# Kernel tuning notes

Hardware: AMD Instinct MI355X
Metric: run time of the kernel (lower is better)

## Reference

```python
import jax, jax.numpy as jnp
import numpy as np

NUM_HEADS = 16
DIM_EMBED = 1024
DIM_CROSS = 768
DIM_HEAD = DIM_EMBED // NUM_HEADS


def setup_inputs() -> dict:
    key = jax.random.key(0)
    ks = jax.random.split(key, 10)
    B, Sq, Skv = 16, 4096, 77
    s_e = 1.0 / np.sqrt(DIM_EMBED)
    s_c = 1.0 / np.sqrt(DIM_CROSS)
    return {
        "x": jax.random.normal(ks[0], (B, Sq, DIM_EMBED), jnp.float32),
        "y": jax.random.normal(ks[1], (B, Skv, DIM_CROSS), jnp.float32),
        "wq": jax.random.uniform(ks[2], (DIM_EMBED, DIM_EMBED), jnp.float32, -s_e, s_e),
        "bq": jax.random.uniform(ks[3], (DIM_EMBED,), jnp.float32, -s_e, s_e),
        "wk": jax.random.uniform(ks[4], (DIM_CROSS, DIM_EMBED), jnp.float32, -s_c, s_c),
        "bk": jax.random.uniform(ks[5], (DIM_EMBED,), jnp.float32, -s_c, s_c),
        "wv": jax.random.uniform(ks[6], (DIM_CROSS, DIM_EMBED), jnp.float32, -s_c, s_c),
        "bv": jax.random.uniform(ks[7], (DIM_EMBED,), jnp.float32, -s_c, s_c),
        "wo": jax.random.uniform(ks[8], (DIM_EMBED, DIM_EMBED), jnp.float32, -s_e, s_e),
        "bo": jax.random.uniform(ks[9], (DIM_EMBED,), jnp.float32, -s_e, s_e),
    }


def reference(x, y, wq, bq, wk, bk, wv, bv, wo, bo):
    B, Sq, E = x.shape
    H, D = NUM_HEADS, DIM_HEAD
    q = (x @ wq + bq).reshape(B, Sq, H, D).transpose(0, 2, 1, 3)   # [B,H,Sq,D]
    k = (y @ wk + bk).reshape(B, -1, H, D).transpose(0, 2, 1, 3)   # [B,H,Skv,D]
    v = (y @ wv + bv).reshape(B, -1, H, D).transpose(0, 2, 1, 3)   # [B,H,Skv,D]
    scale = 1.0 / jnp.sqrt(jnp.asarray(D, dtype=q.dtype))
    scores = jnp.einsum("bhqd,bhkd->bhqk", q, k) * scale           # [B,H,Sq,Skv]
    attn = jax.nn.softmax(scores, axis=-1)
    out = jnp.einsum("bhqk,bhkd->bhqd", attn, v)                   # [B,H,Sq,D]
    out = out.transpose(0, 2, 1, 3).reshape(B, Sq, E)
    return out @ wo + bo
```

## Files before the change

kernel.cpp:

```cpp
#include <hip/hip_runtime.h>

typedef unsigned short u16;
typedef __attribute__((ext_vector_type(4))) float f32x4;
typedef __attribute__((ext_vector_type(8))) short bf16x8;
typedef __attribute__((ext_vector_type(8))) unsigned short u16x8;
typedef __attribute__((ext_vector_type(4))) unsigned short u16x4;

__device__ __forceinline__ u16 f2bf(float f) {
  union { float f; unsigned u; } v; v.f = f;
  unsigned r = v.u + 0x7FFFu + ((v.u >> 16) & 1u);
  return (u16)(r >> 16);
}
__device__ __forceinline__ float bf2f(u16 h) {
  union { unsigned u; float f; } v; v.u = ((unsigned)h) << 16; return v.f;
}

__device__ __forceinline__ void gload_lds16(const void* g, void* l) {
  __builtin_amdgcn_global_load_lds((const __attribute__((address_space(1))) void*)g,
                                   (__attribute__((address_space(3))) void*)l, 16, 0, 0);
}


__global__ void k_zero(u16x8* __restrict__ p, int n8) {
  int i = blockIdx.x * blockDim.x + threadIdx.x;
  int stride = gridDim.x * blockDim.x;
  u16x8 z = (u16x8)0;
  for (; i < n8; i += stride) p[i] = z;
}

__global__ void k_cvt_x(const float* __restrict__ in, u16* __restrict__ out, int n4) {
  int i = blockIdx.x * blockDim.x + threadIdx.x;
  int stride = gridDim.x * blockDim.x;
  const f32x4* in4 = (const f32x4*)in;
  u16x4* out4 = (u16x4*)out;
  for (; i < n4; i += stride) {
    f32x4 v = in4[i];
    u16x4 o;
    o[0] = f2bf(v[0]); o[1] = f2bf(v[1]); o[2] = f2bf(v[2]); o[3] = f2bf(v[3]);
    out4[i] = o;
  }
}

__global__ void k_prep_wt(const float* __restrict__ wq, const float* __restrict__ wo,
                          const float* __restrict__ wk, const float* __restrict__ wv,
                          u16* __restrict__ WQ1T, u16* __restrict__ WO1T,
                          u16* __restrict__ WK1T, u16* __restrict__ WV1T) {
  __shared__ u16 tile[64][72];
  int bid = blockIdx.x;
  const float* w; u16* o; int K;
  if (bid < 256)      { w = wq; o = WQ1T; K = 1024; }
  else if (bid < 512) { w = wo; o = WO1T; K = 1024; bid -= 256; }
  else if (bid < 704) { w = wk; o = WK1T; K = 768;  bid -= 512; }
  else                { w = wv; o = WV1T; K = 768;  bid -= 704; }
  const int ti = bid >> 4, tj = bid & 15;
  const int t = threadIdx.x;
  const int r = t >> 2, cq = (t & 3) * 16;

  const float* src = w + (size_t)(ti * 64 + r) * 1024 + tj * 64 + cq;
#pragma unroll
  for (int j4 = 0; j4 < 4; ++j4) {
    f32x4 v = *(const f32x4*)(src + j4 * 4);
#pragma unroll
    for (int e = 0; e < 4; ++e) tile[r][cq + j4 * 4 + e] = f2bf(v[e]);
  }
  __syncthreads();

  u16 vals[16];
#pragma unroll
  for (int j = 0; j < 16; ++j) vals[j] = tile[cq + j][r];
  u16* dst = o + (size_t)(tj * 64 + r) * K + ti * 64 + cq;
  *(u16x8*)dst = *(u16x8*)&vals[0];
  *(u16x8*)(dst + 8) = *(u16x8*)&vals[8];
}

__global__ void k_prep_y(const float* __restrict__ y, u16* __restrict__ yb, int n4) {
  int i = blockIdx.x * blockDim.x + threadIdx.x;
  int stride = gridDim.x * blockDim.x;
  const f32x4* in4 = (const f32x4*)y;
  u16x4* out4 = (u16x4*)yb;
  for (; i < n4; i += stride) {
    f32x4 v = in4[i];
    u16x4 o;
    o[0] = f2bf(v[0]); o[1] = f2bf(v[1]); o[2] = f2bf(v[2]); o[3] = f2bf(v[3]);
    out4[i] = o;
  }
}

__global__ __launch_bounds__(256, 2) void k_gemm_kv(
    const u16* __restrict__ A,
    const u16* __restrict__ BK1, const float* __restrict__ bkb, u16* __restrict__ KTo,
    const u16* __restrict__ BV1, const float* __restrict__ bvb, u16* __restrict__ VTo)
{
  const int M = 1232, Kdim = 768;
  __shared__ u16 sA[128 * 32];
  __shared__ u16 sB[128 * 32];
  const int t = threadIdx.x;
  const int half = blockIdx.x >= 80;
  const int bb = blockIdx.x - half * 80;
  const u16* B = half ? BV1 : BK1;
  const float* bias = half ? bvb : bkb;
  u16* outp = half ? VTo : KTo;
  const int bm = bb / 8, bn = bb % 8;
  const int m0 = bm * 128, n0 = bn * 128;
  const int l = t & 63, wv_ = t >> 6;
  const int lr = l & 15, lg = l >> 4;
  const int wm = (wv_ >> 1) * 64, wn = (wv_ & 1) * 64;

  const int srow = t >> 2;
  const int ssw = ((t >> 2) & 3) ^ ((t >> 4) & 3);
  const int scol = ((t & 3) ^ ssw) * 8;
  char* ldsA = (char*)sA;
  char* ldsB = (char*)sB;
  const int ldsoff = wv_ * 1024;

  const int swl = (lr & 3) ^ ((lr >> 2) & 3);
  const int rds = (lg ^ swl) * 8;

  f32x4 acc[4][4] = {};

  for (int kt = 0; kt < Kdim / 32; ++kt) {
    const int k0 = kt * 32;
    __syncthreads();
    {
      int r1 = m0 + srow;       if (r1 > M - 1) r1 = M - 1;
      int r2 = m0 + 64 + srow;  if (r2 > M - 1) r2 = M - 1;
      gload_lds16(A + (size_t)r1 * Kdim + k0 + scol, ldsA + 0    + ldsoff);
      gload_lds16(A + (size_t)r2 * Kdim + k0 + scol, ldsA + 4096 + ldsoff);
      gload_lds16(B + (size_t)(n0 + srow) * Kdim + k0 + scol,      ldsB + 0    + ldsoff);
      gload_lds16(B + (size_t)(n0 + 64 + srow) * Kdim + k0 + scol, ldsB + 4096 + ldsoff);
    }
    __syncthreads();
    bf16x8 af[4], bfr[4];
#pragma unroll
    for (int mt = 0; mt < 4; ++mt)
      af[mt] = *(const bf16x8*)&sA[(wm + mt * 16 + lr) * 32 + rds];
#pragma unroll
    for (int nt = 0; nt < 4; ++nt)
      bfr[nt] = *(const bf16x8*)&sB[(wn + nt * 16 + lr) * 32 + rds];
#pragma unroll
    for (int mt = 0; mt < 4; ++mt)
#pragma unroll
      for (int nt = 0; nt < 4; ++nt)
        acc[mt][nt] = __builtin_amdgcn_mfma_f32_16x16x32_bf16(af[mt], bfr[nt], acc[mt][nt], 0, 0, 0);
  }

#pragma unroll
  for (int mt = 0; mt < 4; ++mt) {
#pragma unroll
    for (int nt = 0; nt < 4; ++nt) {
      const int gc = n0 + wn + nt * 16 + lr;
      const float bb2 = bias[gc];
#pragma unroll
      for (int r = 0; r < 4; ++r) {
        const int gr = m0 + wm + mt * 16 + lg * 4 + r;
        const float v = acc[mt][nt][r] + bb2;
        if (gr < M) {
          int bI = gr / 77, s = gr - bI * 77;
          int hh = gc >> 6, d = gc & 63;
          if (!half)
            outp[(((size_t)bI * 16 + hh) * 96 + s) * 64 + d] = f2bf(v);
          else
            outp[(((size_t)bI * 16 + hh) * 64 + d) * 96 + s] = f2bf(v);
        }
      }
    }
  }
}

template <int EPI>
__global__ __launch_bounds__(512, 2) void gemm256(
    const u16* __restrict__ A, const u16* __restrict__ Bp,
    const float* __restrict__ bias, void* __restrict__ outp,
    const u16* __restrict__ KT, const u16* __restrict__ VT)
{
  __shared__ char lds[131072];
  const int t = threadIdx.x;
  const int cpx = (int)gridDim.x >> 3;
  const int swz = ((int)blockIdx.x & 7) * cpx + ((int)blockIdx.x >> 3);
  const int bm = swz >> 2, bn = swz & 3;
  const int m0 = bm * 256, n0 = bn * 256;
  const int w = t >> 6, l = t & 63, lr = l & 15, lg = l >> 4;
  const int wm = w >> 2, wn = w & 3;

  const int srow = t >> 2;
  const int scol = ((t & 3) ^ ((t >> 2) & 3) ^ ((t >> 4) & 3)) * 8;
  const int rsw = (lg ^ (lr & 3) ^ ((lr >> 2) & 3)) << 4;
  const int arow = wm * 128 + lr;
  const int brow = wn * 64 + lr;

  f32x4 acc[8][4] = {};

#define RD(dstA, dstB, sbb) { \
  _Pragma("unroll") for (int q = 0; q < 8; ++q) \
    dstA[q] = *(const bf16x8*)(lds + (sbb) + ((arow + q * 16) << 6) + rsw); \
  _Pragma("unroll") for (int nt = 0; nt < 4; ++nt) \
    dstB[nt] = *(const bf16x8*)(lds + (sbb) + 16384 + ((brow + nt * 16) << 6) + rsw); }
#define STAGE(kt, sbb) { \
    gload_lds16(A  + (size_t)(m0 + srow) * 1024 + (kt) * 32 + scol,       lds + (sbb) + t * 16); \
    gload_lds16(A  + (size_t)(m0 + 128 + srow) * 1024 + (kt) * 32 + scol, lds + (sbb) + 8192 + t * 16); \
    gload_lds16(Bp + (size_t)(n0 + srow) * 1024 + (kt) * 32 + scol,       lds + (sbb) + 16384 + t * 16); \
    gload_lds16(Bp + (size_t)(n0 + 128 + srow) * 1024 + (kt) * 32 + scol, lds + (sbb) + 24576 + t * 16); }
#define MM(a_, b_) { __builtin_amdgcn_s_setprio(1); \
  _Pragma("unroll") for (int q = 0; q < 8; ++q) \
    _Pragma("unroll") for (int nt = 0; nt < 4; ++nt) \
      acc[q][nt] = __builtin_amdgcn_mfma_f32_16x16x32_bf16(a_[q], b_[nt], acc[q][nt], 0, 0, 0); \
  __builtin_amdgcn_s_setprio(0); }
#define BAR __builtin_amdgcn_s_barrier()
#define SB0 __builtin_amdgcn_sched_barrier(0)
#define VM8 asm volatile("s_waitcnt vmcnt(8)" ::: "memory")

  bf16x8 aA[8], bA[4], aB[8], bB[4];

  STAGE(0, 0); STAGE(1, 32768); STAGE(2, 65536);
  VM8; SB0; BAR;
  RD(aA, bA, 0);

  int rdo = 32768, sto = 98304;
#pragma unroll 1
  for (int tt = 0; tt < 32; tt += 2) {
    {
      int ks = tt + 3; if (ks > 31) ks = 31;
      STAGE(ks, sto); sto = (sto + 32768) & 131071;
      VM8; SB0; BAR;
      RD(aB, bB, rdo); rdo = (rdo + 32768) & 131071;
      MM(aA, bA);
      BAR;
    }
    {
      int ks = tt + 4; if (ks > 31) ks = 31;
      STAGE(ks, sto); sto = (sto + 32768) & 131071;
      VM8; SB0; BAR;
      RD(aA, bA, rdo); rdo = (rdo + 32768) & 131071;
      MM(aB, bB);
      BAR;
    }
  }
  asm volatile("s_waitcnt vmcnt(0)" ::: "memory");
  SB0; BAR;

#undef RD
#undef STAGE
#undef MM
#undef BAR
#undef SB0
#undef VM8

  if constexpr (EPI == 1) {
#pragma unroll
    for (int q = 0; q < 8; ++q) {
#pragma unroll
      for (int nt = 0; nt < 4; ++nt) {
        const int gc = n0 + wn * 64 + nt * 16 + lr;
        const float bb = bias[gc];
#pragma unroll
        for (int r = 0; r < 4; ++r) {
          const int gr = m0 + wm * 128 + q * 16 + lg * 4 + r;
          ((float*)outp)[(size_t)gr * 1024 + gc] = acc[q][nt][r] + bb;
        }
      }
    }
  } else {
    const int hh = (n0 >> 6) + wn;
    const int b = m0 >> 12;
    const u16* gK = KT + (size_t)(b * 16 + hh) * (96 * 64);
    const u16* gV = VT + (size_t)(b * 16 + hh) * (64 * 96);
    u16* Qs = (u16*)(lds + w * 16384);
    u16* Ps = (u16*)(lds + w * 16384 + 8192);
    u16* QBo = (u16*)outp;

    bf16x8 fk[5][2], fv[4][3];
#pragma unroll
    for (int nt = 0; nt < 5; ++nt)
#pragma unroll
      for (int ks = 0; ks < 2; ++ks)
        fk[nt][ks] = *(const bf16x8*)&gK[(nt * 16 + lr) * 64 + ks * 32 + lg * 8];
#pragma unroll
    for (int nt = 0; nt < 4; ++nt)
#pragma unroll
      for (int ks = 0; ks < 3; ++ks)
        fv[nt][ks] = *(const bf16x8*)&gV[(nt * 16 + lr) * 96 + ks * 32 + lg * 8];

    float bb[4];
#pragma unroll
    for (int nt = 0; nt < 4; ++nt) bb[nt] = bias[n0 + wn * 64 + nt * 16 + lr];

#pragma unroll
    for (int cc = 0; cc < 4; ++cc) {
#pragma unroll
      for (int qq = 0; qq < 2; ++qq)
#pragma unroll
        for (int nt = 0; nt < 4; ++nt)
#pragma unroll
          for (int r = 0; r < 4; ++r)
            Qs[(qq * 16 + lg * 4 + r) * 72 + nt * 16 + lr] =
                f2bf(acc[cc * 2 + qq][nt][r] + bb[nt]);

      bf16x8 aq[2][2];
#pragma unroll
      for (int qq = 0; qq < 2; ++qq)
#pragma unroll
        for (int ks = 0; ks < 2; ++ks)
          aq[qq][ks] = *(const bf16x8*)&Qs[(qq * 16 + lr) * 72 + ks * 32 + lg * 8];

      f32x4 s_[2][5] = {};
#pragma unroll
      for (int nt = 0; nt < 5; ++nt)
#pragma unroll
        for (int ks = 0; ks < 2; ++ks)
#pragma unroll
          for (int qq = 0; qq < 2; ++qq)
            s_[qq][nt] = __builtin_amdgcn_mfma_f32_16x16x32_bf16(aq[qq][ks], fk[nt][ks], s_[qq][nt], 0, 0, 0);
#pragma unroll
      for (int qq = 0; qq < 2; ++qq)
#pragma unroll
        for (int nt = 0; nt < 5; ++nt)
#pragma unroll
          for (int r = 0; r < 4; ++r)
            s_[qq][nt][r] *= 0.125f;
      if (lr >= 13) {
#pragma unroll
        for (int qq = 0; qq < 2; ++qq)
#pragma unroll
          for (int r = 0; r < 4; ++r)
            s_[qq][4][r] = -1e30f;
      }

      float ri[2][4];
#pragma unroll
      for (int qq = 0; qq < 2; ++qq) {
#pragma unroll
        for (int r = 0; r < 4; ++r) {
          float m1 = s_[qq][0][r];
#pragma unroll
          for (int nt = 1; nt < 5; ++nt) m1 = fmaxf(m1, s_[qq][nt][r]);
          m1 = fmaxf(m1, __shfl_xor(m1, 1, 64));
          m1 = fmaxf(m1, __shfl_xor(m1, 2, 64));
          m1 = fmaxf(m1, __shfl_xor(m1, 4, 64));
          m1 = fmaxf(m1, __shfl_xor(m1, 8, 64));
          float s1 = 0.f;
#pragma unroll
          for (int nt = 0; nt < 5; ++nt) {
            float e = __expf(s_[qq][nt][r] - m1);
            s_[qq][nt][r] = e;
            s1 += e;
          }
          s1 += __shfl_xor(s1, 1, 64);
          s1 += __shfl_xor(s1, 2, 64);
          s1 += __shfl_xor(s1, 4, 64);
          s1 += __shfl_xor(s1, 8, 64);
          ri[qq][r] = 1.0f / s1;
        }
      }

#pragma unroll
      for (int qq = 0; qq < 2; ++qq)
#pragma unroll
        for (int nt = 0; nt < 5; ++nt)
#pragma unroll
          for (int r = 0; r < 4; ++r)
            Ps[(qq * 16 + lg * 4 + r) * 104 + nt * 16 + lr] = f2bf(s_[qq][nt][r] * ri[qq][r]);
#pragma unroll
      for (int qq = 0; qq < 2; ++qq)
#pragma unroll
        for (int r = 0; r < 4; ++r)
          Ps[(qq * 16 + lg * 4 + r) * 104 + 80 + lr] = 0;

      f32x4 o_[2][4] = {};
#pragma unroll
      for (int ks = 0; ks < 3; ++ks) {
        bf16x8 ap[2];
#pragma unroll
        for (int qq = 0; qq < 2; ++qq)
          ap[qq] = *(const bf16x8*)&Ps[(qq * 16 + lr) * 104 + ks * 32 + lg * 8];
#pragma unroll
        for (int nt = 0; nt < 4; ++nt)
#pragma unroll
          for (int qq = 0; qq < 2; ++qq)
            o_[qq][nt] = __builtin_amdgcn_mfma_f32_16x16x32_bf16(ap[qq], fv[nt][ks], o_[qq][nt], 0, 0, 0);
      }

#pragma unroll
      for (int qq = 0; qq < 2; ++qq)
#pragma unroll
        for (int nt = 0; nt < 4; ++nt)
#pragma unroll
          for (int r = 0; r < 4; ++r)
            QBo[(size_t)(m0 + wm * 128 + cc * 32 + qq * 16 + lg * 4 + r) * 1024
                + hh * 64 + nt * 16 + lr] = f2bf(o_[qq][nt][r]);
    }
  }
}


extern "C" void kernel_launch(void* const* d_in, const int* in_sizes, int n_in,
                              void* d_out, int out_size, void* d_ws, size_t ws_size,
                              hipStream_t stream) {
  const float* x  = (const float*)d_in[0];
  const float* y  = (const float*)d_in[1];
  const float* wq = (const float*)d_in[2];
  const float* bq = (const float*)d_in[3];
  const float* wk = (const float*)d_in[4];
  const float* bk = (const float*)d_in[5];
  const float* wv = (const float*)d_in[6];
  const float* bv = (const float*)d_in[7];
  const float* wo = (const float*)d_in[8];
  const float* bo = (const float*)d_in[9];

  char* ws = (char*)d_ws;
  u16* QB   = (u16*)(ws + 0);
  u16* WQ1T = (u16*)(ws + 134217728);
  u16* WO1T = (u16*)(ws + 136314880);
  u16* WK1T = (u16*)(ws + 138412032);
  u16* WV1T = (u16*)(ws + 139984896);
  u16* YB   = (u16*)(ws + 141557760);
  u16* KT   = (u16*)(ws + 143654912);
  u16* VT   = (u16*)(ws + 146800640);

  u16*   XB  = (u16*)d_out;
  float* OUT = (float*)d_out;

  k_zero<<<768, 256, 0, stream>>>((u16x8*)KT, 393216);
  k_cvt_x<<<4096, 256, 0, stream>>>(x, XB, 16777216);
  k_prep_wt<<<896, 256, 0, stream>>>(wq, wo, wk, wv, WQ1T, WO1T, WK1T, WV1T);
  k_prep_y<<<924, 256, 0, stream>>>(y, YB, 236544);

  k_gemm_kv<<<160, 256, 0, stream>>>(YB, WK1T, bk, KT, WV1T, bv, VT);

  gemm256<0><<<1024, 512, 0, stream>>>(XB, WQ1T, bq, QB, KT, VT);

  gemm256<1><<<1024, 512, 0, stream>>>(QB, WO1T, bo, OUT, nullptr, nullptr);
}
```

Baseline: 531.9 us.

## Restructure GEMM main loop into 8-phase ping-pong with BK=64 double buffering

The 256x256 GEMM main loop changes from a 4-deep ring of BK=32 stages to two 64 KB buffers holding BK=64 tiles. Each K-chunk is split into four phases that interleave partial LDS reads, global-to-LDS loads for the next chunk, and 16-MFMA groups, with barriers between phases. The LDS row stride becomes 128 bytes with an 8-way XOR swizzle. The goal is finer overlap of memory traffic with MFMA work and fewer loop iterations, at the cost of more barriers per chunk and a shallower prefetch depth.

```diff
diff --git a/kernel.cpp b/kernel.cpp
--- a/kernel.cpp
+++ b/kernel.cpp
@@ -168,7 +168,7 @@
 }
 
 template <int EPI>
-__global__ __launch_bounds__(512, 2) void gemm256(
+__global__ __launch_bounds__(512, 2) void gemm8p(
     const u16* __restrict__ A, const u16* __restrict__ Bp,
     const float* __restrict__ bias, void* __restrict__ outp,
     const u16* __restrict__ KT, const u16* __restrict__ VT)
@@ -182,68 +182,77 @@
   const int w = t >> 6, l = t & 63, lr = l & 15, lg = l >> 4;
   const int wm = w >> 2, wn = w & 3;
 
-  const int srow = t >> 2;
-  const int scol = ((t & 3) ^ ((t >> 2) & 3) ^ ((t >> 4) & 3)) * 8;
-  const int rsw = (lg ^ (lr & 3) ^ ((lr >> 2) & 3)) << 4;
-  const int arow = wm * 128 + lr;
-  const int brow = wn * 64 + lr;
+  const int srow = t >> 3;
+  const int scol = ((t & 7) ^ ((t >> 3) & 7)) << 3;
+  const int sw0 = ((lg) ^ (lr & 7)) << 4;
+  const int sw1 = ((4 + lg) ^ (lr & 7)) << 4;
+  const int abase = wm * 128 + lr;
+  const int bbase = wn * 64 + lr;
 
   f32x4 acc[8][4] = {};
 
-#define RD(dstA, dstB, sbb) { \
-  _Pragma("unroll") for (int q = 0; q < 8; ++q) \
-    dstA[q] = *(const bf16x8*)(lds + (sbb) + ((arow + q * 16) << 6) + rsw); \
-  _Pragma("unroll") for (int nt = 0; nt < 4; ++nt) \
-    dstB[nt] = *(const bf16x8*)(lds + (sbb) + 16384 + ((brow + nt * 16) << 6) + rsw); }
-#define STAGE(kt, sbb) { \
-    gload_lds16(A  + (size_t)(m0 + srow) * 1024 + (kt) * 32 + scol,       lds + (sbb) + t * 16); \
-    gload_lds16(A  + (size_t)(m0 + 128 + srow) * 1024 + (kt) * 32 + scol, lds + (sbb) + 8192 + t * 16); \
-    gload_lds16(Bp + (size_t)(n0 + srow) * 1024 + (kt) * 32 + scol,       lds + (sbb) + 16384 + t * 16); \
-    gload_lds16(Bp + (size_t)(n0 + 128 + srow) * 1024 + (kt) * 32 + scol, lds + (sbb) + 24576 + t * 16); }
-#define MM(a_, b_) { __builtin_amdgcn_s_setprio(1); \
-  _Pragma("unroll") for (int q = 0; q < 8; ++q) \
+#define RD_A(dst, db, mh, ksw) { _Pragma("unroll") for (int q = 0; q < 4; ++q) \
+    dst[q] = *(const bf16x8*)(lds + (db) + ((abase + (mh) * 64 + q * 16) << 7) + (ksw)); }
+#define RD_B(dst, db, ksw) { _Pragma("unroll") for (int nt = 0; nt < 4; ++nt) \
+    dst[nt] = *(const bf16x8*)(lds + (db) + 32768 + ((bbase + nt * 16) << 7) + (ksw)); }
+#define STG_A(kt, dn, j) gload_lds16(A + (size_t)(m0 + (j) * 64 + srow) * 1024 + (kt) * 64 + scol, \
+                                     lds + (dn) + (j) * 8192 + t * 16)
+#define STG_B(kt, dn, j) gload_lds16(Bp + (size_t)(n0 + (j) * 64 + srow) * 1024 + (kt) * 64 + scol, \
+                                     lds + (dn) + 32768 + (j) * 8192 + t * 16)
+#define MM16(ab, a_, b_) { __builtin_amdgcn_s_setprio(1); \
+  _Pragma("unroll") for (int q = 0; q < 4; ++q) \
     _Pragma("unroll") for (int nt = 0; nt < 4; ++nt) \
-      acc[q][nt] = __builtin_amdgcn_mfma_f32_16x16x32_bf16(a_[q], b_[nt], acc[q][nt], 0, 0, 0); \
+      acc[(ab) + q][nt] = __builtin_amdgcn_mfma_f32_16x16x32_bf16(a_[q], b_[nt], acc[(ab) + q][nt], 0, 0, 0); \
   __builtin_amdgcn_s_setprio(0); }
 #define BAR __builtin_amdgcn_s_barrier()
 #define SB0 __builtin_amdgcn_sched_barrier(0)
-#define VM8 asm volatile("s_waitcnt vmcnt(8)" ::: "memory")
-
-  bf16x8 aA[8], bA[4], aB[8], bB[4];
-
-  STAGE(0, 0); STAGE(1, 32768); STAGE(2, 65536);
-  VM8; SB0; BAR;
-  RD(aA, bA, 0);
-
-  int rdo = 32768, sto = 98304;
-#pragma unroll 1
-  for (int tt = 0; tt < 32; tt += 2) {
-    {
-      int ks = tt + 3; if (ks > 31) ks = 31;
-      STAGE(ks, sto); sto = (sto + 32768) & 131071;
-      VM8; SB0; BAR;
-      RD(aB, bB, rdo); rdo = (rdo + 32768) & 131071;
-      MM(aA, bA);
-      BAR;
-    }
-    {
-      int ks = tt + 4; if (ks > 31) ks = 31;
-      STAGE(ks, sto); sto = (sto + 32768) & 131071;
-      VM8; SB0; BAR;
-      RD(aA, bA, rdo); rdo = (rdo + 32768) & 131071;
-      MM(aB, bB);
-      BAR;
-    }
+#define VM2 asm volatile("s_waitcnt vmcnt(2)" ::: "memory")
+#define VM4 asm volatile("s_waitcnt vmcnt(4)" ::: "memory")
+
+  STG_B(0, 0, 0); STG_B(0, 0, 1);
+  STG_A(0, 0, 0); STG_A(0, 0, 2);
+  STG_B(0, 0, 2); STG_B(0, 0, 3);
+  STG_A(0, 0, 1); STG_A(0, 0, 3);
+  VM2; SB0; BAR;
+
+#pragma unroll 2
+  for (int c = 0; c < 16; ++c) {
+    const int db = (c & 1) * 65536, dn = db ^ 65536;
+    int cn = c + 1; if (cn > 15) cn = 15;
+    bf16x8 a_[4], b0[4], b1[4];
+    RD_A(a_, db, 0, sw0); RD_B(b0, db, sw0);
+    STG_B(cn, dn, 0); STG_B(cn, dn, 1);
+    BAR;
+    MM16(0, a_, b0);
+    BAR;
+    RD_A(a_, db, 0, sw1); RD_B(b1, db, sw1);
+    STG_A(cn, dn, 0); STG_A(cn, dn, 2);
+    VM4; SB0; BAR;
+    MM16(0, a_, b1);
+    BAR;
+    RD_A(a_, db, 1, sw0);
+    STG_B(cn, dn, 2); STG_B(cn, dn, 3);
+    BAR;
+    MM16(4, a_, b0);
+    BAR;
+    RD_A(a_, db, 1, sw1);
+    STG_A(cn, dn, 1); STG_A(cn, dn, 3);
+    VM2; SB0; BAR;
+    MM16(4, a_, b1);
+    BAR;
   }
   asm volatile("s_waitcnt vmcnt(0)" ::: "memory");
   SB0; BAR;
 
-#undef RD
-#undef STAGE
-#undef MM
+#undef RD_A
+#undef RD_B
+#undef STG_A
+#undef STG_B
+#undef MM16
 #undef BAR
 #undef SB0
-#undef VM8
+#undef VM2
+#undef VM4
 
   if constexpr (EPI == 1) {
 #pragma unroll
@@ -426,7 +435,7 @@
 
   k_gemm_kv<<<160, 256, 0, stream>>>(YB, WK1T, bk, KT, WV1T, bv, VT);
 
-  gemm256<0><<<1024, 512, 0, stream>>>(XB, WQ1T, bq, QB, KT, VT);
-
-  gemm256<1><<<1024, 512, 0, stream>>>(QB, WO1T, bo, OUT, nullptr, nullptr);
-}
+  gemm8p<0><<<1024, 512, 0, stream>>>(XB, WQ1T, bq, QB, KT, VT);
+
+  gemm8p<1><<<1024, 512, 0, stream>>>(QB, WO1T, bo, OUT, nullptr, nullptr);
+}
```

New measurement: 490.3 us (median of 2 runs). 7.8% less time.
